# Performance work log

Measured on AMD Instinct MI355X. Metric: run time of the kernel, lower is better.

The kernel has to match this reference:

```python
import jax, jax.numpy as jnp
import numpy as np

D = 1024
H = 16
HD = D // H
SCALE = np.sqrt(HD).astype(np.float32)


def setup_inputs() -> dict:
    key = jax.random.key(0)
    ks = jax.random.split(key, 12)
    s = lambda fan_in: 1.0 / np.sqrt(fan_in)
    return {
        "x": jax.random.normal(ks[0], (4, 2048, D), dtype=jnp.float32),
        "qkv_w": jax.random.uniform(ks[1], (D, 3 * D), jnp.float32, -s(D), s(D)),
        "qkv_b": jax.random.uniform(ks[2], (3 * D,), jnp.float32, -s(D), s(D)),
        "out_w": jax.random.uniform(ks[3], (D, D), jnp.float32, -s(D), s(D)),
        "out_b": jax.random.uniform(ks[4], (D,), jnp.float32, -s(D), s(D)),
        "ln1_g": jnp.ones((D,), jnp.float32),
        "ln1_b": jnp.zeros((D,), jnp.float32),
        "ln2_g": jnp.ones((D,), jnp.float32),
        "ln2_b": jnp.zeros((D,), jnp.float32),
        "ffn_w1": jax.random.uniform(ks[5], (D, 4 * D), jnp.float32, -s(D), s(D)),
        "ffn_b1": jax.random.uniform(ks[6], (4 * D,), jnp.float32, -s(D), s(D)),
        "ffn_w2": jax.random.uniform(ks[7], (4 * D, D), jnp.float32, -s(4 * D), s(4 * D)),
        "ffn_b2": jax.random.uniform(ks[8], (D,), jnp.float32, -s(4 * D), s(4 * D)),
    }


def _layer_norm(x, g, b, eps=1e-5):
    mu = jnp.mean(x, axis=-1, keepdims=True)
    var = jnp.mean(jnp.square(x - mu), axis=-1, keepdims=True)
    return (x - mu) * jax.lax.rsqrt(var + eps) * g + b


def reference(x, qkv_w, qkv_b, out_w, out_b, ln1_g, ln1_b, ln2_g, ln2_b,
              ffn_w1, ffn_b1, ffn_w2, ffn_b2):
    B, L, C = x.shape
    h = _layer_norm(x, ln1_g, ln1_b)
    qkv = (h @ qkv_w + qkv_b).reshape(B, L, 3, H, HD)
    q = jnp.transpose(qkv[:, :, 0], (0, 2, 1, 3))  # [B,H,L,HD]
    k = jnp.transpose(qkv[:, :, 1], (0, 2, 1, 3))
    v = jnp.transpose(qkv[:, :, 2], (0, 2, 1, 3))
    attn = jnp.einsum("bhqd,bhkd->bhqk", q, k) / SCALE
    attn = jax.nn.softmax(attn, axis=-1)
    o = jnp.einsum("bhqk,bhkd->bhqd", attn, v)
    o = jnp.transpose(o, (0, 2, 1, 3)).reshape(B, L, C)
    o = o @ out_w + out_b
    out = _layer_norm(o, ln2_g, ln2_b)
    ffn = jax.nn.gelu(out @ ffn_w1 + ffn_b1, approximate=False) @ ffn_w2 + ffn_b2
    return out + ffn
```

## Files before the change

### kernel.cpp

```cpp
#include <hip/hip_runtime.h>
#include <hip/hip_bf16.h>
#include <math.h>

typedef __bf16 bf16_t;
typedef __bf16 bf16x8 __attribute__((ext_vector_type(8)));
typedef __bf16 bf16x4 __attribute__((ext_vector_type(4)));
typedef float  f32x4  __attribute__((ext_vector_type(4)));

#define MFMA_BF16(a, b, c) __builtin_amdgcn_mfma_f32_16x16x32_bf16(a, b, c, 0, 0, 0)

#if __has_builtin(__builtin_amdgcn_exp2f)
__device__ __forceinline__ float fast_exp2(float x) { return __builtin_amdgcn_exp2f(x); }
#else
__device__ __forceinline__ float fast_exp2(float x) { return exp2f(x); }
#endif

__device__ __forceinline__ float fast_gelu(float v) {
  const float u = v * (1.f + 0.044715f * v * v);
  const float tt = fast_exp2(2.3022078f * u);
  return v - v / (tt + 1.f);
}

__device__ __forceinline__ void gload_lds16(const bf16_t* g, bf16_t* l) {
  __builtin_amdgcn_global_load_lds(
      (const __attribute__((address_space(1))) void*)g,
      (__attribute__((address_space(3))) void*)l, 16, 0, 0);
}

__global__ __launch_bounds__(256) void sa_transpose(const float* __restrict__ in,
                                                    bf16_t* __restrict__ out,
                                                    int K, int N) {
  __shared__ bf16_t tile[64][65];
  const int n0 = blockIdx.x * 64, k0 = blockIdx.y * 64;
  const int t = threadIdx.x;
#pragma unroll
  for (int i = 0; i < 16; ++i) {
    int idx = t + i * 256;
    int r = idx >> 6, c = idx & 63;
    tile[r][c] = (bf16_t)in[(size_t)(k0 + r) * N + n0 + c];
  }
  __syncthreads();
#pragma unroll
  for (int i = 0; i < 16; ++i) {
    int idx = t + i * 256;
    int r = idx >> 6, c = idx & 63;
    out[(size_t)(n0 + r) * K + k0 + c] = tile[c][r];
  }
}

__global__ __launch_bounds__(256) void sa_layernorm(const float* __restrict__ in,
                                                    const float* __restrict__ gamma,
                                                    const float* __restrict__ beta,
                                                    bf16_t* __restrict__ out_bf,
                                                    float* __restrict__ out_f) {
  const int row = blockIdx.x, t = threadIdx.x;
  const float4 v = *(const float4*)(in + (size_t)row * 1024 + t * 4);
  float s  = v.x + v.y + v.z + v.w;
  float ss = v.x * v.x + v.y * v.y + v.z * v.z + v.w * v.w;
#pragma unroll
  for (int m = 1; m < 64; m <<= 1) {
    s  += __shfl_xor(s, m, 64);
    ss += __shfl_xor(ss, m, 64);
  }
  __shared__ float red[8];
  const int w = t >> 6, lane = t & 63;
  if (lane == 0) { red[w] = s; red[4 + w] = ss; }
  __syncthreads();
  s  = red[0] + red[1] + red[2] + red[3];
  ss = red[4] + red[5] + red[6] + red[7];
  const float mu   = s * (1.f / 1024.f);
  const float rstd = rsqrtf(ss * (1.f / 1024.f) - mu * mu + 1e-5f);
  const float4 gv = *(const float4*)(gamma + t * 4);
  const float4 bv = *(const float4*)(beta + t * 4);
  const float y0 = (v.x - mu) * rstd * gv.x + bv.x;
  const float y1 = (v.y - mu) * rstd * gv.y + bv.y;
  const float y2 = (v.z - mu) * rstd * gv.z + bv.z;
  const float y3 = (v.w - mu) * rstd * gv.w + bv.w;
  bf16x4 ob = { (bf16_t)y0, (bf16_t)y1, (bf16_t)y2, (bf16_t)y3 };
  *(bf16x4*)(out_bf + (size_t)row * 1024 + t * 4) = ob;
  if (out_f) {
    float4 of = { y0, y1, y2, y3 };
    *(float4*)(out_f + (size_t)row * 1024 + t * 4) = of;
  }
}

__global__ __launch_bounds__(256) void sa_layernorm_b(const bf16_t* __restrict__ in,
                                                      const float* __restrict__ gamma,
                                                      const float* __restrict__ beta,
                                                      bf16_t* __restrict__ out_bf) {
  const int row = blockIdx.x, t = threadIdx.x;
  const bf16x4 iv = *(const bf16x4*)(in + (size_t)row * 1024 + t * 4);
  const float v0 = (float)iv[0], v1 = (float)iv[1], v2 = (float)iv[2], v3 = (float)iv[3];
  float s  = v0 + v1 + v2 + v3;
  float ss = v0 * v0 + v1 * v1 + v2 * v2 + v3 * v3;
#pragma unroll
  for (int m = 1; m < 64; m <<= 1) {
    s  += __shfl_xor(s, m, 64);
    ss += __shfl_xor(ss, m, 64);
  }
  __shared__ float red[8];
  const int w = t >> 6, lane = t & 63;
  if (lane == 0) { red[w] = s; red[4 + w] = ss; }
  __syncthreads();
  s  = red[0] + red[1] + red[2] + red[3];
  ss = red[4] + red[5] + red[6] + red[7];
  const float mu   = s * (1.f / 1024.f);
  const float rstd = rsqrtf(ss * (1.f / 1024.f) - mu * mu + 1e-5f);
  const float4 gv = *(const float4*)(gamma + t * 4);
  const float4 bv = *(const float4*)(beta + t * 4);
  bf16x4 ob = { (bf16_t)((v0 - mu) * rstd * gv.x + bv.x),
                (bf16_t)((v1 - mu) * rstd * gv.y + bv.y),
                (bf16_t)((v2 - mu) * rstd * gv.z + bv.z),
                (bf16_t)((v3 - mu) * rstd * gv.w + bv.w) };
  *(bf16x4*)(out_bf + (size_t)row * 1024 + t * 4) = ob;
}

template <int EPI>
__global__ __launch_bounds__(256, 2) void sa_gemm4(const bf16_t* __restrict__ A,
                                                   const bf16_t* __restrict__ Bt,
                                                   const float* __restrict__ bias,
                                                   int K, int N,
                                                   float* __restrict__ fout,
                                                   bf16_t* __restrict__ bfout,
                                                   const bf16_t* __restrict__ res,
                                                   bf16_t* __restrict__ qb,
                                                   bf16_t* __restrict__ kb,
                                                   bf16_t* __restrict__ vb) {
  __shared__ __attribute__((aligned(16))) bf16_t As[2][128][64];
  __shared__ __attribute__((aligned(16))) bf16_t Bs[2][128][64];

  const int nwg = gridDim.x * gridDim.y;
  const int flat = blockIdx.y * gridDim.x + blockIdx.x;
  const int wg = (flat & 7) * (nwg >> 3) + (flat >> 3);
  const int bx = wg % gridDim.x, by = wg / gridDim.x;

  const int m0 = by * 128, n0 = bx * 128;
  const int t = threadIdx.x;
  const int w = t >> 6, lane = t & 63;
  const int wr = w >> 1, wc = w & 1;
  const int fr = lane & 15, fq = lane >> 4;
  const int swz = fr & 7;
  const int srow = lane >> 3;
  const int scol = ((lane & 7) ^ srow) * 8;
  const int NT = K >> 6;

  const f32x4 fzero = { 0.f, 0.f, 0.f, 0.f };
  f32x4 acc[4][4];
#pragma unroll
  for (int mi = 0; mi < 4; ++mi)
#pragma unroll
    for (int ni = 0; ni < 4; ++ni) acc[mi][ni] = fzero;

  auto stage = [&](int tt, int sb) {
#pragma unroll
    for (int i = 0; i < 4; ++i) {
      const int c = w * 4 + i;
      const int row = c * 8 + srow;
      gload_lds16(A  + (size_t)(m0 + row) * K + tt * 64 + scol, &As[sb][c * 8][0]);
      gload_lds16(Bt + (size_t)(n0 + row) * K + tt * 64 + scol, &Bs[sb][c * 8][0]);
    }
  };

  stage(0, 0);
  __syncthreads();

  for (int tt = 0; tt < NT; ++tt) {
    const int cur = tt & 1;
    if (tt + 1 < NT) stage(tt + 1, cur ^ 1);

    bf16x8 af[4][2], bfr[4][2];
#pragma unroll
    for (int mi = 0; mi < 4; ++mi)
#pragma unroll
      for (int kk = 0; kk < 2; ++kk)
        af[mi][kk] = *(const bf16x8*)&As[cur][wr * 64 + mi * 16 + fr][((kk * 4 + fq) ^ swz) * 8];
#pragma unroll
    for (int ni = 0; ni < 4; ++ni)
#pragma unroll
      for (int kk = 0; kk < 2; ++kk)
        bfr[ni][kk] = *(const bf16x8*)&Bs[cur][wc * 64 + ni * 16 + fr][((kk * 4 + fq) ^ swz) * 8];

    __builtin_amdgcn_s_setprio(1);
#pragma unroll
    for (int kk = 0; kk < 2; ++kk)
#pragma unroll
      for (int mi = 0; mi < 4; ++mi)
#pragma unroll
        for (int ni = 0; ni < 4; ++ni)
          acc[mi][ni] = MFMA_BF16(af[mi][kk], bfr[ni][kk], acc[mi][ni]);
    __builtin_amdgcn_s_setprio(0);

    __syncthreads();
  }

#pragma unroll
  for (int ni = 0; ni < 4; ++ni) {
    const int n = n0 + wc * 64 + ni * 16 + fr;
    const float bn = bias[n];
#pragma unroll
    for (int mi = 0; mi < 4; ++mi) {
      const int mbase = m0 + wr * 64 + mi * 16 + fq * 4;
      float vv[4];
#pragma unroll
      for (int r = 0; r < 4; ++r) vv[r] = acc[mi][ni][r] + bn;
      if constexpr (EPI == 0) {
        const int which = n >> 10;
        const int hh = (n >> 6) & 15;
        const int d = n & 63;
        const int b = mbase >> 11, l = mbase & 2047;
        if (which == 0) {
#pragma unroll
          for (int r = 0; r < 4; ++r)
            qb[((size_t)(b * 16 + hh) * 2048 + l + r) * 64 + d] =
                (bf16_t)(vv[r] * (0.125f * 1.44269504088896340736f));
        } else if (which == 1) {
#pragma unroll
          for (int r = 0; r < 4; ++r)
            kb[((size_t)(b * 16 + hh) * 2048 + l + r) * 64 + d] = (bf16_t)vv[r];
        } else {
          bf16x4 pv = { (bf16_t)vv[0], (bf16_t)vv[1], (bf16_t)vv[2], (bf16_t)vv[3] };
          *(bf16x4*)(vb + ((size_t)(b * 16 + hh) * 64 + d) * 2048 + l) = pv;
        }
      } else if constexpr (EPI == 1) {
#pragma unroll
        for (int r = 0; r < 4; ++r)
          bfout[(size_t)(mbase + r) * N + n] = (bf16_t)vv[r];
      } else if constexpr (EPI == 2) {
#pragma unroll
        for (int r = 0; r < 4; ++r)
          bfout[(size_t)(mbase + r) * N + n] = (bf16_t)fast_gelu(vv[r]);
      } else {
#pragma unroll
        for (int r = 0; r < 4; ++r)
          fout[(size_t)(mbase + r) * N + n] = vv[r] + (float)res[(size_t)(mbase + r) * N + n];
      }
    }
  }
}

__global__ __launch_bounds__(256) void sa_attn(const bf16_t* __restrict__ qb,
                                               const bf16_t* __restrict__ kb,
                                               const bf16_t* __restrict__ vb,
                                               bf16_t* __restrict__ out) {
  __shared__ __attribute__((aligned(16))) bf16_t Ks[64][64];
  __shared__ __attribute__((aligned(16))) bf16_t Vt[64][64];
  __shared__ __attribute__((aligned(16))) bf16_t Ps[4][16][64];

  const int nwg = gridDim.x * gridDim.y;
  const int flat = blockIdx.y * gridDim.x + blockIdx.x;
  const int wg = (flat & 7) * (nwg >> 3) + (flat >> 3);
  const int qblk = wg & 31, bh = wg >> 5;

  const int t = threadIdx.x, w = t >> 6, lane = t & 63;
  const int fr = lane & 15, fq = lane >> 4;
  const int fx = fr & 7;
  const size_t base = (size_t)bh * 2048 * 64;
  const f32x4 fzero = { 0.f, 0.f, 0.f, 0.f };

  const int row0 = t >> 3;
  const int u0 = t & 7;
  const int sc = (u0 ^ (row0 & 7)) * 8;
  const int gc = u0 * 8;

  *(bf16x8*)&Ks[row0][sc] =
      *(const bf16x8*)(qb + base + (size_t)(qblk * 64 + row0) * 64 + gc);
  *(bf16x8*)&Ks[row0 + 32][sc] =
      *(const bf16x8*)(qb + base + (size_t)(qblk * 64 + row0 + 32) * 64 + gc);

  bf16x8 kreg0, kreg1, vreg0, vreg1;
  kreg0 = *(const bf16x8*)(kb + base + (size_t)row0 * 64 + gc);
  kreg1 = *(const bf16x8*)(kb + base + (size_t)(row0 + 32) * 64 + gc);
  vreg0 = *(const bf16x8*)(vb + base + (size_t)row0 * 2048 + gc);
  vreg1 = *(const bf16x8*)(vb + base + (size_t)(row0 + 32) * 2048 + gc);

  __syncthreads();
  bf16x8 qf[2];
  qf[0] = *(const bf16x8*)&Ks[w * 16 + fr][((0 * 4 + fq) ^ fx) * 8];
  qf[1] = *(const bf16x8*)&Ks[w * 16 + fr][((1 * 4 + fq) ^ fx) * 8];

  f32x4 o_acc[4];
#pragma unroll
  for (int dt = 0; dt < 4; ++dt) o_acc[dt] = fzero;
  f32x4 l4 = fzero;

  for (int kv0 = 0; kv0 < 2048; kv0 += 64) {
    __syncthreads();
    *(bf16x8*)&Ks[row0][sc] = kreg0;
    *(bf16x8*)&Ks[row0 + 32][sc] = kreg1;
    *(bf16x8*)&Vt[row0][sc] = vreg0;
    *(bf16x8*)&Vt[row0 + 32][sc] = vreg1;
    if (kv0 + 64 < 2048) {
      const int kvn = kv0 + 64;
      kreg0 = *(const bf16x8*)(kb + base + (size_t)(kvn + row0) * 64 + gc);
      kreg1 = *(const bf16x8*)(kb + base + (size_t)(kvn + row0 + 32) * 64 + gc);
      vreg0 = *(const bf16x8*)(vb + base + (size_t)row0 * 2048 + kvn + gc);
      vreg1 = *(const bf16x8*)(vb + base + (size_t)(row0 + 32) * 2048 + kvn + gc);
    }
    __syncthreads();

    f32x4 s[4];
#pragma unroll
    for (int kvt = 0; kvt < 4; ++kvt) s[kvt] = fzero;
    __builtin_amdgcn_s_setprio(1);
#pragma unroll
    for (int kk = 0; kk < 2; ++kk) {
#pragma unroll
      for (int kvt = 0; kvt < 4; ++kvt) {
        bf16x8 kf = *(const bf16x8*)&Ks[kvt * 16 + fr][((kk * 4 + fq) ^ fx) * 8];
        s[kvt] = MFMA_BF16(kf, qf[kk], s[kvt]);
      }
    }
    __builtin_amdgcn_s_setprio(0);

#pragma unroll
    for (int kvt = 0; kvt < 4; ++kvt) {
#pragma unroll
      for (int r = 0; r < 4; ++r) s[kvt][r] = fast_exp2(s[kvt][r]);
      l4 += s[kvt];
      bf16x4 pr = { (bf16_t)s[kvt][0], (bf16_t)s[kvt][1],
                    (bf16_t)s[kvt][2], (bf16_t)s[kvt][3] };
      *(bf16x4*)&Ps[w][fr][(((kvt * 2 + (fq >> 1)) ^ fx) * 8) + (fq & 1) * 4] = pr;
    }

    __builtin_amdgcn_s_setprio(1);
#pragma unroll
    for (int ks = 0; ks < 2; ++ks) {
      bf16x8 pf = *(const bf16x8*)&Ps[w][fr][((ks * 4 + fq) ^ fx) * 8];
#pragma unroll
      for (int dt = 0; dt < 4; ++dt) {
        bf16x8 vf = *(const bf16x8*)&Vt[dt * 16 + fr][((ks * 4 + fq) ^ fx) * 8];
        o_acc[dt] = MFMA_BF16(vf, pf, o_acc[dt]);
      }
    }
    __builtin_amdgcn_s_setprio(0);
  }

  float l_run = l4[0] + l4[1] + l4[2] + l4[3];
  l_run += __shfl_xor(l_run, 16, 64);
  l_run += __shfl_xor(l_run, 32, 64);
  const float linv = 1.f / l_run;
  const int b = bh >> 4, h = bh & 15;
  const int qg = qblk * 64 + w * 16 + fr;
#pragma unroll
  for (int dt = 0; dt < 4; ++dt) {
    bf16x4 ov;
#pragma unroll
    for (int r = 0; r < 4; ++r) ov[r] = (bf16_t)(o_acc[dt][r] * linv);
    const int d = dt * 16 + fq * 4;
    *(bf16x4*)(out + ((size_t)(b * 2048 + qg)) * 1024 + h * 64 + d) = ov;
  }
}

extern "C" void kernel_launch(void* const* d_in, const int* in_sizes, int n_in,
                              void* d_out, int out_size, void* d_ws, size_t ws_size,
                              hipStream_t stream) {
  const float* x      = (const float*)d_in[0];
  const float* qkv_w  = (const float*)d_in[1];
  const float* qkv_b  = (const float*)d_in[2];
  const float* out_w  = (const float*)d_in[3];
  const float* out_b  = (const float*)d_in[4];
  const float* ln1_g  = (const float*)d_in[5];
  const float* ln1_b  = (const float*)d_in[6];
  const float* ln2_g  = (const float*)d_in[7];
  const float* ln2_b  = (const float*)d_in[8];
  const float* ffn_w1 = (const float*)d_in[9];
  const float* ffn_b1 = (const float*)d_in[10];
  const float* ffn_w2 = (const float*)d_in[11];
  const float* ffn_b2 = (const float*)d_in[12];
  float* outp = (float*)d_out;

  char* p = (char*)d_ws;
  auto alloc = [&](size_t bytes) { char* r = p; p += bytes; return r; };
  bf16_t* qkvw_t = (bf16_t*)alloc((size_t)3072 * 1024 * 2);
  bf16_t* outw_t = (bf16_t*)alloc((size_t)1024 * 1024 * 2);
  bf16_t* w1_t   = (bf16_t*)alloc((size_t)4096 * 1024 * 2);
  bf16_t* w2_t   = (bf16_t*)alloc((size_t)1024 * 4096 * 2);
  bf16_t* h_bf   = (bf16_t*)alloc((size_t)8192 * 1024 * 2);
  bf16_t* q_buf  = (bf16_t*)alloc((size_t)8192 * 1024 * 2);
  bf16_t* k_buf  = (bf16_t*)alloc((size_t)8192 * 1024 * 2);
  bf16_t* v_buf  = (bf16_t*)alloc((size_t)8192 * 1024 * 2);
  bf16_t* a_bf   = (bf16_t*)alloc((size_t)8192 * 1024 * 2);
  bf16_t* o_bf   = (bf16_t*)alloc((size_t)8192 * 1024 * 2);
  bf16_t* out_bf = (bf16_t*)alloc((size_t)8192 * 1024 * 2);
  bf16_t* t_bf   = (bf16_t*)alloc((size_t)8192 * 4096 * 2);

  sa_transpose<<<dim3(3072 / 64, 1024 / 64), 256, 0, stream>>>(qkv_w, qkvw_t, 1024, 3072);
  sa_transpose<<<dim3(1024 / 64, 1024 / 64), 256, 0, stream>>>(out_w, outw_t, 1024, 1024);
  sa_transpose<<<dim3(4096 / 64, 1024 / 64), 256, 0, stream>>>(ffn_w1, w1_t, 1024, 4096);
  sa_transpose<<<dim3(1024 / 64, 4096 / 64), 256, 0, stream>>>(ffn_w2, w2_t, 4096, 1024);

  sa_layernorm<<<8192, 256, 0, stream>>>(x, ln1_g, ln1_b, h_bf, nullptr);

  sa_gemm4<0><<<dim3(3072 / 128, 8192 / 128), 256, 0, stream>>>(
      h_bf, qkvw_t, qkv_b, 1024, 3072, nullptr, nullptr, nullptr, q_buf, k_buf, v_buf);

  sa_attn<<<dim3(32, 64), 256, 0, stream>>>(q_buf, k_buf, v_buf, a_bf);

  sa_gemm4<1><<<dim3(1024 / 128, 8192 / 128), 256, 0, stream>>>(
      a_bf, outw_t, out_b, 1024, 1024, nullptr, o_bf, nullptr, nullptr, nullptr, nullptr);

  sa_layernorm_b<<<8192, 256, 0, stream>>>(o_bf, ln2_g, ln2_b, out_bf);

  sa_gemm4<2><<<dim3(4096 / 128, 8192 / 128), 256, 0, stream>>>(
      out_bf, w1_t, ffn_b1, 1024, 4096, nullptr, t_bf, nullptr, nullptr, nullptr, nullptr);

  sa_gemm4<3><<<dim3(1024 / 128, 8192 / 128), 256, 0, stream>>>(
      t_bf, w2_t, ffn_b2, 4096, 1024, outp, nullptr, out_bf, nullptr, nullptr, nullptr);
}
```

Measured before the change: 395.2 us.

## Widen GEMM tile to 128x256 with triple-buffered interleaved load pipeline

```diff
diff --git a/kernel.cpp b/kernel.cpp
--- a/kernel.cpp
+++ b/kernel.cpp
@@ -116,7 +116,7 @@
 }
 
 template <int EPI>
-__global__ __launch_bounds__(256, 2) void sa_gemm4(const bf16_t* __restrict__ A,
+__global__ __launch_bounds__(512, 1) void sa_gemm5(const bf16_t* __restrict__ A,
                                                    const bf16_t* __restrict__ Bt,
                                                    const float* __restrict__ bias,
                                                    int K, int N,
@@ -126,18 +126,18 @@
                                                    bf16_t* __restrict__ qb,
                                                    bf16_t* __restrict__ kb,
                                                    bf16_t* __restrict__ vb) {
-  __shared__ __attribute__((aligned(16))) bf16_t As[2][128][64];
-  __shared__ __attribute__((aligned(16))) bf16_t Bs[2][128][64];
+  __shared__ __attribute__((aligned(16))) bf16_t As[3][128][64];
+  __shared__ __attribute__((aligned(16))) bf16_t Bs[3][256][64];
 
   const int nwg = gridDim.x * gridDim.y;
   const int flat = blockIdx.y * gridDim.x + blockIdx.x;
   const int wg = (flat & 7) * (nwg >> 3) + (flat >> 3);
   const int bx = wg % gridDim.x, by = wg / gridDim.x;
 
-  const int m0 = by * 128, n0 = bx * 128;
+  const int m0 = by * 128, n0 = bx * 256;
   const int t = threadIdx.x;
-  const int w = t >> 6, lane = t & 63;
-  const int wr = w >> 1, wc = w & 1;
+  const int wid = t >> 6, lane = t & 63;
+  const int wm = wid >> 2, wn = wid & 3;
   const int fr = lane & 15, fq = lane >> 4;
   const int swz = fr & 7;
   const int srow = lane >> 3;
@@ -151,55 +151,105 @@
 #pragma unroll
     for (int ni = 0; ni < 4; ++ni) acc[mi][ni] = fzero;
 
-  auto stage = [&](int tt, int sb) {
-#pragma unroll
-    for (int i = 0; i < 4; ++i) {
-      const int c = w * 4 + i;
-      const int row = c * 8 + srow;
-      gload_lds16(A  + (size_t)(m0 + row) * K + tt * 64 + scol, &As[sb][c * 8][0]);
-      gload_lds16(Bt + (size_t)(n0 + row) * K + tt * 64 + scol, &Bs[sb][c * 8][0]);
-    }
+  auto stA = [&](int tt, int sb, int i) {
+    const int ch = wid * 2 + i;
+    gload_lds16(A + (size_t)(m0 + ch * 8 + srow) * K + tt * 64 + scol,
+                &As[sb][ch * 8][0]);
   };
-
-  stage(0, 0);
-  __syncthreads();
+  auto stB = [&](int tt, int sb, int i) {
+    const int ch = wid * 4 + i;
+    gload_lds16(Bt + (size_t)(n0 + ch * 8 + srow) * K + tt * 64 + scol,
+                &Bs[sb][ch * 8][0]);
+  };
+
+  stA(0, 0, 0); stA(0, 0, 1); stB(0, 0, 0); stB(0, 0, 1); stB(0, 0, 2); stB(0, 0, 3);
+  stA(1, 1, 0); stA(1, 1, 1); stB(1, 1, 0); stB(1, 1, 1); stB(1, 1, 2); stB(1, 1, 3);
+  asm volatile("s_waitcnt vmcnt(6)" ::: "memory");
+  __builtin_amdgcn_s_barrier();
 
   for (int tt = 0; tt < NT; ++tt) {
-    const int cur = tt & 1;
-    if (tt + 1 < NT) stage(tt + 1, cur ^ 1);
-
-    bf16x8 af[4][2], bfr[4][2];
-#pragma unroll
-    for (int mi = 0; mi < 4; ++mi)
+    const int cur = tt % 3;
+    const int nxt = (tt + 2) % 3;
+    const bool st = (tt + 2) < NT;
+    bf16x8 bfr[4][2], af0[2], af1[2], af2[2], af3[2];
+
+#pragma unroll
+    for (int ni = 0; ni < 4; ++ni)
 #pragma unroll
       for (int kk = 0; kk < 2; ++kk)
-        af[mi][kk] = *(const bf16x8*)&As[cur][wr * 64 + mi * 16 + fr][((kk * 4 + fq) ^ swz) * 8];
-#pragma unroll
-    for (int ni = 0; ni < 4; ++ni)
-#pragma unroll
-      for (int kk = 0; kk < 2; ++kk)
-        bfr[ni][kk] = *(const bf16x8*)&Bs[cur][wc * 64 + ni * 16 + fr][((kk * 4 + fq) ^ swz) * 8];
-
-    __builtin_amdgcn_s_setprio(1);
-#pragma unroll
-    for (int kk = 0; kk < 2; ++kk)
-#pragma unroll
-      for (int mi = 0; mi < 4; ++mi)
-#pragma unroll
-        for (int ni = 0; ni < 4; ++ni)
-          acc[mi][ni] = MFMA_BF16(af[mi][kk], bfr[ni][kk], acc[mi][ni]);
-    __builtin_amdgcn_s_setprio(0);
-
-    __syncthreads();
+        bfr[ni][kk] = *(const bf16x8*)&Bs[cur][wn * 64 + ni * 16 + fr][((kk * 4 + fq) ^ swz) * 8];
+#pragma unroll
+    for (int kk = 0; kk < 2; ++kk)
+      af0[kk] = *(const bf16x8*)&As[cur][wm * 64 + 0 * 16 + fr][((kk * 4 + fq) ^ swz) * 8];
+    if (st) { stA(tt + 2, nxt, 0); stA(tt + 2, nxt, 1); }
+    __builtin_amdgcn_s_barrier();
+    asm volatile("s_waitcnt lgkmcnt(0)" ::: "memory");
+    __builtin_amdgcn_s_setprio(1);
+#pragma unroll
+    for (int kk = 0; kk < 2; ++kk)
+#pragma unroll
+      for (int ni = 0; ni < 4; ++ni)
+        acc[0][ni] = MFMA_BF16(af0[kk], bfr[ni][kk], acc[0][ni]);
+    __builtin_amdgcn_s_setprio(0);
+    __builtin_amdgcn_s_barrier();
+
+#pragma unroll
+    for (int kk = 0; kk < 2; ++kk)
+      af1[kk] = *(const bf16x8*)&As[cur][wm * 64 + 1 * 16 + fr][((kk * 4 + fq) ^ swz) * 8];
+    if (st) { stB(tt + 2, nxt, 0); stB(tt + 2, nxt, 1); }
+    __builtin_amdgcn_s_barrier();
+    asm volatile("s_waitcnt lgkmcnt(0)" ::: "memory");
+    __builtin_amdgcn_s_setprio(1);
+#pragma unroll
+    for (int kk = 0; kk < 2; ++kk)
+#pragma unroll
+      for (int ni = 0; ni < 4; ++ni)
+        acc[1][ni] = MFMA_BF16(af1[kk], bfr[ni][kk], acc[1][ni]);
+    __builtin_amdgcn_s_setprio(0);
+    __builtin_amdgcn_s_barrier();
+
+#pragma unroll
+    for (int kk = 0; kk < 2; ++kk)
+      af2[kk] = *(const bf16x8*)&As[cur][wm * 64 + 2 * 16 + fr][((kk * 4 + fq) ^ swz) * 8];
+    if (st) stB(tt + 2, nxt, 2);
+    __builtin_amdgcn_s_barrier();
+    asm volatile("s_waitcnt lgkmcnt(0)" ::: "memory");
+    __builtin_amdgcn_s_setprio(1);
+#pragma unroll
+    for (int kk = 0; kk < 2; ++kk)
+#pragma unroll
+      for (int ni = 0; ni < 4; ++ni)
+        acc[2][ni] = MFMA_BF16(af2[kk], bfr[ni][kk], acc[2][ni]);
+    __builtin_amdgcn_s_setprio(0);
+    __builtin_amdgcn_s_barrier();
+
+#pragma unroll
+    for (int kk = 0; kk < 2; ++kk)
+      af3[kk] = *(const bf16x8*)&As[cur][wm * 64 + 3 * 16 + fr][((kk * 4 + fq) ^ swz) * 8];
+    if (st) stB(tt + 2, nxt, 3);
+    __builtin_amdgcn_s_barrier();
+    asm volatile("s_waitcnt lgkmcnt(0)" ::: "memory");
+    __builtin_amdgcn_s_setprio(1);
+#pragma unroll
+    for (int kk = 0; kk < 2; ++kk)
+#pragma unroll
+      for (int ni = 0; ni < 4; ++ni)
+        acc[3][ni] = MFMA_BF16(af3[kk], bfr[ni][kk], acc[3][ni]);
+    __builtin_amdgcn_s_setprio(0);
+    if (tt + 1 < NT) {
+      if (st) asm volatile("s_waitcnt vmcnt(6)" ::: "memory");
+      else    asm volatile("s_waitcnt vmcnt(0)" ::: "memory");
+    }
+    __builtin_amdgcn_s_barrier();
   }
 
 #pragma unroll
   for (int ni = 0; ni < 4; ++ni) {
-    const int n = n0 + wc * 64 + ni * 16 + fr;
+    const int n = n0 + wn * 64 + ni * 16 + fr;
     const float bn = bias[n];
 #pragma unroll
     for (int mi = 0; mi < 4; ++mi) {
-      const int mbase = m0 + wr * 64 + mi * 16 + fq * 4;
+      const int mbase = m0 + wm * 64 + mi * 16 + fq * 4;
       float vv[4];
 #pragma unroll
       for (int r = 0; r < 4; ++r) vv[r] = acc[mi][ni][r] + bn;
@@ -391,19 +441,19 @@
 
   sa_layernorm<<<8192, 256, 0, stream>>>(x, ln1_g, ln1_b, h_bf, nullptr);
 
-  sa_gemm4<0><<<dim3(3072 / 128, 8192 / 128), 256, 0, stream>>>(
+  sa_gemm5<0><<<dim3(3072 / 256, 8192 / 128), 512, 0, stream>>>(
       h_bf, qkvw_t, qkv_b, 1024, 3072, nullptr, nullptr, nullptr, q_buf, k_buf, v_buf);
 
   sa_attn<<<dim3(32, 64), 256, 0, stream>>>(q_buf, k_buf, v_buf, a_bf);
 
-  sa_gemm4<1><<<dim3(1024 / 128, 8192 / 128), 256, 0, stream>>>(
+  sa_gemm5<1><<<dim3(1024 / 256, 8192 / 128), 512, 0, stream>>>(
       a_bf, outw_t, out_b, 1024, 1024, nullptr, o_bf, nullptr, nullptr, nullptr, nullptr);
 
   sa_layernorm_b<<<8192, 256, 0, stream>>>(o_bf, ln2_g, ln2_b, out_bf);
 
-  sa_gemm4<2><<<dim3(4096 / 128, 8192 / 128), 256, 0, stream>>>(
+  sa_gemm5<2><<<dim3(4096 / 256, 8192 / 128), 512, 0, stream>>>(
       out_bf, w1_t, ffn_b1, 1024, 4096, nullptr, t_bf, nullptr, nullptr, nullptr, nullptr);
 
-  sa_gemm4<3><<<dim3(1024 / 128, 8192 / 128), 256, 0, stream>>>(
+  sa_gemm5<3><<<dim3(1024 / 256, 8192 / 128), 512, 0, stream>>>(
       t_bf, w2_t, ffn_b2, 4096, 1024, outp, nullptr, out_bf, nullptr, nullptr, nullptr);
 }
```

New measurement: 473.5 us. 19.8% more time.

## Rewrite attention with 32x32x16 MFMA, 128-query tiles and register-resident P

Applied to the files above, without the earlier changes.

```diff
diff --git a/kernel.cpp b/kernel.cpp
--- a/kernel.cpp
+++ b/kernel.cpp
@@ -6,8 +6,12 @@
 typedef __bf16 bf16x8 __attribute__((ext_vector_type(8)));
 typedef __bf16 bf16x4 __attribute__((ext_vector_type(4)));
 typedef float  f32x4  __attribute__((ext_vector_type(4)));
+typedef float  f32x16 __attribute__((ext_vector_type(16)));
+typedef unsigned int u32x2 __attribute__((ext_vector_type(2)));
+typedef unsigned int u32x4 __attribute__((ext_vector_type(4)));
 
 #define MFMA_BF16(a, b, c) __builtin_amdgcn_mfma_f32_16x16x32_bf16(a, b, c, 0, 0, 0)
+#define MFMA32_BF16(a, b, c) __builtin_amdgcn_mfma_f32_32x32x16_bf16(a, b, c, 0, 0, 0)
 
 #if __has_builtin(__builtin_amdgcn_exp2f)
 __device__ __forceinline__ float fast_exp2(float x) { return __builtin_amdgcn_exp2f(x); }
@@ -238,34 +242,31 @@
   }
 }
 
-__global__ __launch_bounds__(256) void sa_attn(const bf16_t* __restrict__ qb,
-                                               const bf16_t* __restrict__ kb,
-                                               const bf16_t* __restrict__ vb,
-                                               bf16_t* __restrict__ out) {
+__global__ __launch_bounds__(256) void sa_attn32(const bf16_t* __restrict__ qb,
+                                                 const bf16_t* __restrict__ kb,
+                                                 const bf16_t* __restrict__ vb,
+                                                 bf16_t* __restrict__ out) {
   __shared__ __attribute__((aligned(16))) bf16_t Ks[64][64];
   __shared__ __attribute__((aligned(16))) bf16_t Vt[64][64];
-  __shared__ __attribute__((aligned(16))) bf16_t Ps[4][16][64];
 
   const int nwg = gridDim.x * gridDim.y;
   const int flat = blockIdx.y * gridDim.x + blockIdx.x;
   const int wg = (flat & 7) * (nwg >> 3) + (flat >> 3);
-  const int qblk = wg & 31, bh = wg >> 5;
-
-  const int t = threadIdx.x, w = t >> 6, lane = t & 63;
-  const int fr = lane & 15, fq = lane >> 4;
-  const int fx = fr & 7;
+  const int qblk = wg & 15, bh = wg >> 4;
+
+  const int t = threadIdx.x, wq = t >> 6, lane = t & 63;
+  const int q31 = lane & 31, hi = lane >> 5;
+  const int qx = q31 & 7;
   const size_t base = (size_t)bh * 2048 * 64;
-  const f32x4 fzero = { 0.f, 0.f, 0.f, 0.f };
-
-  const int row0 = t >> 3;
-  const int u0 = t & 7;
+
+  const int row0 = t >> 3, u0 = t & 7;
   const int sc = (u0 ^ (row0 & 7)) * 8;
   const int gc = u0 * 8;
 
-  *(bf16x8*)&Ks[row0][sc] =
-      *(const bf16x8*)(qb + base + (size_t)(qblk * 64 + row0) * 64 + gc);
-  *(bf16x8*)&Ks[row0 + 32][sc] =
-      *(const bf16x8*)(qb + base + (size_t)(qblk * 64 + row0 + 32) * 64 + gc);
+  const bf16_t* qrow = qb + base + (size_t)(qblk * 128 + wq * 32 + q31) * 64 + hi * 8;
+  bf16x8 qf[4];
+#pragma unroll
+  for (int c = 0; c < 4; ++c) qf[c] = *(const bf16x8*)(qrow + c * 16);
 
   bf16x8 kreg0, kreg1, vreg0, vreg1;
   kreg0 = *(const bf16x8*)(kb + base + (size_t)row0 * 64 + gc);
@@ -273,15 +274,10 @@
   vreg0 = *(const bf16x8*)(vb + base + (size_t)row0 * 2048 + gc);
   vreg1 = *(const bf16x8*)(vb + base + (size_t)(row0 + 32) * 2048 + gc);
 
-  __syncthreads();
-  bf16x8 qf[2];
-  qf[0] = *(const bf16x8*)&Ks[w * 16 + fr][((0 * 4 + fq) ^ fx) * 8];
-  qf[1] = *(const bf16x8*)&Ks[w * 16 + fr][((1 * 4 + fq) ^ fx) * 8];
-
-  f32x4 o_acc[4];
-#pragma unroll
-  for (int dt = 0; dt < 4; ++dt) o_acc[dt] = fzero;
-  f32x4 l4 = fzero;
+  f32x16 o0, o1;
+#pragma unroll
+  for (int i = 0; i < 16; ++i) { o0[i] = 0.f; o1[i] = 0.f; }
+  float lsum = 0.f;
 
   for (int kv0 = 0; kv0 < 2048; kv0 += 64) {
     __syncthreads();
@@ -298,56 +294,67 @@
     }
     __syncthreads();
 
-    f32x4 s[4];
-#pragma unroll
-    for (int kvt = 0; kvt < 4; ++kvt) s[kvt] = fzero;
+    f32x16 s0, s1;
+#pragma unroll
+    for (int i = 0; i < 16; ++i) { s0[i] = 0.f; s1[i] = 0.f; }
     __builtin_amdgcn_s_setprio(1);
 #pragma unroll
-    for (int kk = 0; kk < 2; ++kk) {
-#pragma unroll
-      for (int kvt = 0; kvt < 4; ++kvt) {
-        bf16x8 kf = *(const bf16x8*)&Ks[kvt * 16 + fr][((kk * 4 + fq) ^ fx) * 8];
-        s[kvt] = MFMA_BF16(kf, qf[kk], s[kvt]);
-      }
+    for (int c = 0; c < 4; ++c) {
+      bf16x8 ka0 = *(const bf16x8*)&Ks[q31]     [((2 * c + hi) ^ qx) * 8];
+      bf16x8 ka1 = *(const bf16x8*)&Ks[q31 + 32][((2 * c + hi) ^ qx) * 8];
+      s0 = MFMA32_BF16(ka0, qf[c], s0);
+      s1 = MFMA32_BF16(ka1, qf[c], s1);
     }
     __builtin_amdgcn_s_setprio(0);
 
 #pragma unroll
-    for (int kvt = 0; kvt < 4; ++kvt) {
-#pragma unroll
-      for (int r = 0; r < 4; ++r) s[kvt][r] = fast_exp2(s[kvt][r]);
-      l4 += s[kvt];
-      bf16x4 pr = { (bf16_t)s[kvt][0], (bf16_t)s[kvt][1],
-                    (bf16_t)s[kvt][2], (bf16_t)s[kvt][3] };
-      *(bf16x4*)&Ps[w][fr][(((kvt * 2 + (fq >> 1)) ^ fx) * 8) + (fq & 1) * 4] = pr;
-    }
+    for (int i = 0; i < 16; ++i) { s0[i] = fast_exp2(s0[i]); lsum += s0[i]; }
+#pragma unroll
+    for (int i = 0; i < 16; ++i) { s1[i] = fast_exp2(s1[i]); lsum += s1[i]; }
+
+    u32x4 pw[4];
+#define PACK_CHUNK(c, SB, off)                                                      \
+    {                                                                               \
+      unsigned int x0, x1, y0, y1;                                                  \
+      asm("v_cvt_pk_bf16_f32 %0, %1, %2" : "=v"(x0) : "v"(SB[off+0]), "v"(SB[off+1])); \
+      asm("v_cvt_pk_bf16_f32 %0, %1, %2" : "=v"(x1) : "v"(SB[off+2]), "v"(SB[off+3])); \
+      asm("v_cvt_pk_bf16_f32 %0, %1, %2" : "=v"(y0) : "v"(SB[off+4]), "v"(SB[off+5])); \
+      asm("v_cvt_pk_bf16_f32 %0, %1, %2" : "=v"(y1) : "v"(SB[off+6]), "v"(SB[off+7])); \
+      u32x2 r0 = __builtin_amdgcn_permlane32_swap(x0, y0, false, false);            \
+      u32x2 r1 = __builtin_amdgcn_permlane32_swap(x1, y1, false, false);            \
+      pw[c][0] = r0[0]; pw[c][1] = r1[0]; pw[c][2] = r0[1]; pw[c][3] = r1[1];       \
+    }
+    PACK_CHUNK(0, s0, 0)
+    PACK_CHUNK(1, s0, 8)
+    PACK_CHUNK(2, s1, 0)
+    PACK_CHUNK(3, s1, 8)
+#undef PACK_CHUNK
 
     __builtin_amdgcn_s_setprio(1);
 #pragma unroll
-    for (int ks = 0; ks < 2; ++ks) {
-      bf16x8 pf = *(const bf16x8*)&Ps[w][fr][((ks * 4 + fq) ^ fx) * 8];
-#pragma unroll
-      for (int dt = 0; dt < 4; ++dt) {
-        bf16x8 vf = *(const bf16x8*)&Vt[dt * 16 + fr][((ks * 4 + fq) ^ fx) * 8];
-        o_acc[dt] = MFMA_BF16(vf, pf, o_acc[dt]);
-      }
+    for (int c = 0; c < 4; ++c) {
+      bf16x8 pf = *(const bf16x8*)&pw[c];
+      bf16x8 va0 = *(const bf16x8*)&Vt[q31]     [((2 * c + hi) ^ qx) * 8];
+      bf16x8 va1 = *(const bf16x8*)&Vt[q31 + 32][((2 * c + hi) ^ qx) * 8];
+      o0 = MFMA32_BF16(va0, pf, o0);
+      o1 = MFMA32_BF16(va1, pf, o1);
     }
     __builtin_amdgcn_s_setprio(0);
   }
 
-  float l_run = l4[0] + l4[1] + l4[2] + l4[3];
-  l_run += __shfl_xor(l_run, 16, 64);
-  l_run += __shfl_xor(l_run, 32, 64);
-  const float linv = 1.f / l_run;
+  lsum += __shfl_xor(lsum, 32, 64);
+  const float linv = 1.f / lsum;
   const int b = bh >> 4, h = bh & 15;
-  const int qg = qblk * 64 + w * 16 + fr;
-#pragma unroll
-  for (int dt = 0; dt < 4; ++dt) {
-    bf16x4 ov;
-#pragma unroll
-    for (int r = 0; r < 4; ++r) ov[r] = (bf16_t)(o_acc[dt][r] * linv);
-    const int d = dt * 16 + fq * 4;
-    *(bf16x4*)(out + ((size_t)(b * 2048 + qg)) * 1024 + h * 64 + d) = ov;
+  const int qg = qblk * 128 + wq * 32 + q31;
+  bf16_t* orow = out + (size_t)(b * 2048 + qg) * 1024 + h * 64;
+#pragma unroll
+  for (int rg = 0; rg < 4; ++rg) {
+    bf16x4 olo = { (bf16_t)(o0[4 * rg + 0] * linv), (bf16_t)(o0[4 * rg + 1] * linv),
+                   (bf16_t)(o0[4 * rg + 2] * linv), (bf16_t)(o0[4 * rg + 3] * linv) };
+    *(bf16x4*)(orow + 8 * rg + 4 * hi) = olo;
+    bf16x4 ohi = { (bf16_t)(o1[4 * rg + 0] * linv), (bf16_t)(o1[4 * rg + 1] * linv),
+                   (bf16_t)(o1[4 * rg + 2] * linv), (bf16_t)(o1[4 * rg + 3] * linv) };
+    *(bf16x4*)(orow + 32 + 8 * rg + 4 * hi) = ohi;
   }
 }
 
@@ -394,7 +401,7 @@
   sa_gemm4<0><<<dim3(3072 / 128, 8192 / 128), 256, 0, stream>>>(
       h_bf, qkvw_t, qkv_b, 1024, 3072, nullptr, nullptr, nullptr, q_buf, k_buf, v_buf);
 
-  sa_attn<<<dim3(32, 64), 256, 0, stream>>>(q_buf, k_buf, v_buf, a_bf);
+  sa_attn32<<<dim3(16, 64), 256, 0, stream>>>(q_buf, k_buf, v_buf, a_bf);
 
   sa_gemm4<1><<<dim3(1024 / 128, 8192 / 128), 256, 0, stream>>>(
       a_bf, outw_t, out_b, 1024, 1024, nullptr, o_bf, nullptr, nullptr, nullptr, nullptr);
```

Result: faster. 384.8 us (-2.6%).
